# Optimization experiments

Measured on AMD Instinct MI355X. Metric: run time of the kernel, lower is better.

Reference implementation:

```python
import jax, jax.numpy as jnp
import numpy as np

NX, NY = 512, 512
DX, DY = 1e-4, 1e-4
VS = 1550.0
DT = 2.5e-8


def setup_inputs() -> dict:
    key = jax.random.key(0)
    k1, k2 = jax.random.split(key)
    sensor_data = jax.random.normal(k1, (4, 2, 128, 2048), dtype=jnp.float32)
    sensor_xy = jax.random.randint(k2, (128, 2), 0, 512, dtype=jnp.int32)
    return {"sensor_data": sensor_data, "sensor_xy": sensor_xy}


def _delay_indices(sensor_xy):
    # pixel grids, 1-indexed as in the torch code (arange(1,513))
    ix = jnp.arange(1, NX + 1, dtype=jnp.float32)[None, :, None]  # (1,Nx,1)
    iy = jnp.arange(1, NY + 1, dtype=jnp.float32)[None, None, :]  # (1,1,Ny)
    x = sensor_xy[:, 0].astype(jnp.float32)[:, None, None]        # (S,1,1)
    y = sensor_xy[:, 1].astype(jnp.float32)[:, None, None]
    dis = jnp.sqrt(((x - ix + 1.0) * DX) ** 2 + ((y - iy + 1.0) * DY) ** 2)  # (S,Nx,Ny)
    # .to(torch.long) truncates; values are non-negative so int cast matches
    return (dis / VS / DT).astype(jnp.int32).reshape(sensor_xy.shape[0], -1)  # (S, Nx*Ny)


def reference(sensor_data, sensor_xy):
    B = sensor_data.shape[0]
    S = sensor_xy.shape[0]
    t = _delay_indices(sensor_xy)                           # (S, P) int32
    data = jnp.transpose(sensor_data, (2, 0, 1, 3))         # (S, B, 2, T)

    def step(img, xs):
        t_s, d_s = xs                                       # (P,), (B,2,T)
        return img + d_s[:, :, t_s], None                   # gather + accumulate

    img0 = jnp.zeros((B, 2, NX * NY), dtype=sensor_data.dtype)
    img, _ = jax.lax.scan(step, img0, (t, data))
    return img.reshape(B, 2, NX, NY)
```

## Files before the change

kernel.cpp:

```cpp
#include <hip/hip_runtime.h>
#include <math.h>


#define NXY 512
#define S_CNT 128
#define T_CNT 2048
#define CH 8
#define CH_STRIDE (S_CNT * T_CNT)
#define NPIX (NXY * NXY)
#define TAB_BYTES (NPIX * 2)
#define CHUNK 32
#define NCHUNK (S_CNT / CHUNK)
#define WIN 64
#define PATW 24
#define PAT_STRIDE (16 * PATW)

#pragma float_control(push)
#pragma float_control(precise, on)
__device__ __forceinline__ unsigned short delay_entry(int adx, int ady) {
    const double DX32 = (double)1e-4f;
    const double R1 = (double)(float)(1.0 / 1550.0);
    const double R2 = (double)(float)(1.0 / (double)2.5e-8f);
    float dxf = (float)((double)adx * DX32);
    float dyf = (float)((double)ady * DX32);
    float a2 = (float)((double)dxf * (double)dxf);
    float b2 = (float)((double)dyf * (double)dyf);
    float sum = (float)((double)a2 + (double)b2);
    float dis = (float)sqrt((double)sum);
    float q1 = (float)((double)dis * R1);
    float q2 = (float)((double)q1 * R2);
    return (unsigned short)(int)q2;
}

__device__ __forceinline__ unsigned int bf16_rne(float f) {
    unsigned int x = __float_as_uint(f);
    return (x + 0x7fffu + ((x >> 16) & 1u)) >> 16;
}

__global__ __launch_bounds__(256) void prep4(const float* __restrict__ data,
                                             unsigned short* __restrict__ tab,
                                             uint4* __restrict__ d2b) {
    int g = blockIdx.x * 256 + threadIdx.x;
    unsigned int t01, t23;
    {
        int i0 = 4 * g;
        t01 = (unsigned int)delay_entry(i0 >> 9, i0 & 511) |
              ((unsigned int)delay_entry((i0 + 1) >> 9, (i0 + 1) & 511) << 16);
        t23 = (unsigned int)delay_entry((i0 + 2) >> 9, (i0 + 2) & 511) |
              ((unsigned int)delay_entry((i0 + 3) >> 9, (i0 + 3) & 511) << 16);
    }
    ((uint2*)tab)[g] = make_uint2(t01, t23);

    const float4* data4 = (const float4*)data;
    float4 v[CH];
#pragma unroll
    for (int ch = 0; ch < CH; ++ch) v[ch] = data4[ch * (CH_STRIDE / 4) + g];
#pragma unroll
    for (int q = 0; q < 4; ++q) {
        const float* e0 = (const float*)&v[0];
        unsigned int w0 = bf16_rne(((const float*)&v[0])[q]) | (bf16_rne(((const float*)&v[1])[q]) << 16);
        unsigned int w1 = bf16_rne(((const float*)&v[2])[q]) | (bf16_rne(((const float*)&v[3])[q]) << 16);
        unsigned int w2 = bf16_rne(((const float*)&v[4])[q]) | (bf16_rne(((const float*)&v[5])[q]) << 16);
        unsigned int w3 = bf16_rne(((const float*)&v[6])[q]) | (bf16_rne(((const float*)&v[7])[q]) << 16);
        d2b[4 * g + q] = make_uint4(w0, w1, w2, w3);
        (void)e0;
    }
}

__device__ __forceinline__ int tmin_entry(int adx, int ady) {
    return (int)delay_entry(adx, ady);
}
#pragma float_control(pop)

__device__ __forceinline__ float bflo(unsigned int u) { return __uint_as_float(u << 16); }
__device__ __forceinline__ float bfhi(unsigned int u) { return __uint_as_float(u & 0xffff0000u); }

__device__ __forceinline__ unsigned int sub16x2(unsigned int a, unsigned int t) {
    unsigned int lo = (a - t) & 0xffffu;
    unsigned int hi = ((a >> 16) - t) << 16;
    return lo | hi;
}

__global__ __launch_bounds__(256) void das_gather_ilp(const uint4* __restrict__ d2b,
                                                      const unsigned short* __restrict__ tab,
                                                      const int* __restrict__ sxy,
                                                      float* __restrict__ out) {
    __shared__ uint2 minfo[S_CNT];
    __shared__ uint2 mstage[S_CNT];
    __shared__ uint4 winb[CHUNK * WIN];
    __shared__ uint4 patb[CHUNK * 16 * 3];
    const unsigned short* pat16 = (const unsigned short*)patb;

    int tid = threadIdx.x;
    int x0 = (blockIdx.x >> 5) << 4;
    int y0 = (blockIdx.x & 31) << 4;

    if (tid < S_CNT) {
        int sxv = sxy[2 * tid];
        int syv = sxy[2 * tid + 1];
        int axm = sxv < x0 ? x0 - sxv : (sxv > x0 + 15 ? sxv - x0 - 15 : 0);
        int aym = syv < y0 ? y0 - syv : (syv > y0 + 15 ? syv - y0 - 15 : 0);
        int ay0 = aym & ~7;
        int tmin = tmin_entry(axm, aym);
        minfo[tid] = make_uint2((unsigned int)(sxv | (syv << 16)),
                                (unsigned int)(axm * PATW + ay0));
        mstage[tid] = make_uint2((unsigned int)(axm | (ay0 << 16)), (unsigned int)tmin);
    }
    __syncthreads();

    int iy = y0 | (((tid >> 6) & 1) << 3) | (tid & 7);
    int ix = x0 | ((tid >> 7) << 3) | ((tid >> 3) & 7);

    float acc[CH];
#pragma unroll
    for (int k = 0; k < CH; ++k) acc[k] = 0.0f;

    for (int c = 0; c < NCHUNK; ++c) {
        int s0 = c * CHUNK;

        {
            int lsw = tid >> 3;
            int tm = (int)mstage[s0 + lsw].y;
            const uint4* src = d2b + ((s0 + lsw) << 11) + tm;
            int e0 = tid & 7;
#pragma unroll
            for (int j = 0; j < 8; ++j)
                winb[(lsw << 6) + e0 + 8 * j] = src[e0 + 8 * j];
        }

#pragma unroll
        for (int j = 0; j < 6; ++j) {
            unsigned int idx = (unsigned int)tid + 256u * j;
            unsigned int r3 = idx / 3u;
            unsigned int cc = idx - r3 * 3u;
            unsigned int row = r3 & 15u;
            unsigned int ls = r3 >> 4;
            uint2 st = mstage[s0 + ls];
            int ax0 = (int)(st.x & 0xffffu);
            int ay0 = (int)(st.x >> 16);
            unsigned int tm = st.y;
            const uint4* src = (const uint4*)((const char*)tab +
                (((size_t)(ax0 + (int)row) << 10) + ((size_t)ay0 << 1) + ((size_t)cc << 4)));
            uint4 v = *src;
            v.x = sub16x2(v.x, tm);
            v.y = sub16x2(v.y, tm);
            v.z = sub16x2(v.z, tm);
            v.w = sub16x2(v.w, tm);
            patb[ls * 48u + row * 3u + cc] = v;
        }
        __syncthreads();

        unsigned int tw[CHUNK];
#pragma unroll
        for (int ls = 0; ls < CHUNK; ++ls) {
            uint2 mi = minfo[s0 + ls];
            int sxv = (int)(mi.x & 0xffffu);
            int syv = (int)(mi.x >> 16);
            int dxi = sxv - ix;
            int dyi = syv - iy;
            int adx = dxi < 0 ? -dxi : dxi;
            int ady = dyi < 0 ? -dyi : dyi;
            int pidx = adx * PATW + ady - (int)mi.y;
            tw[ls] = (unsigned int)pat16[ls * PAT_STRIDE + pidx];
        }

#pragma unroll
        for (int ls = 0; ls < CHUNK; ++ls) {
            uint4 w = winb[(ls << 6) + tw[ls]];
            acc[0] += bflo(w.x);
            acc[1] += bfhi(w.x);
            acc[2] += bflo(w.y);
            acc[3] += bfhi(w.y);
            acc[4] += bflo(w.z);
            acc[5] += bfhi(w.z);
            acc[6] += bflo(w.w);
            acc[7] += bfhi(w.w);
        }
        __syncthreads();
    }

    int pix = (ix << 9) | iy;
#pragma unroll
    for (int k = 0; k < CH; ++k) out[k * NPIX + pix] = acc[k];
}

#pragma float_control(push)
#pragma float_control(precise, on)
__global__ __launch_bounds__(256) void build_table(unsigned short* __restrict__ tab) {
    int idx = blockIdx.x * 256 + threadIdx.x;
    tab[idx] = delay_entry(idx >> 9, idx & 511);
}
#pragma float_control(pop)

__global__ __launch_bounds__(256) void das_main(const float* __restrict__ data,
                                                const unsigned short* __restrict__ tab,
                                                const int* __restrict__ sxy,
                                                float* __restrict__ out) {
    __shared__ int sx[S_CNT];
    __shared__ int sy[S_CNT];
    int tid = threadIdx.x;
    if (tid < S_CNT) {
        sx[tid] = sxy[2 * tid];
        sy[tid] = sxy[2 * tid + 1];
    }
    __syncthreads();
    int iy = ((blockIdx.x & 31) << 4) | (tid & 15);
    int ix = ((blockIdx.x >> 5) << 4) | (tid >> 4);
    float acc[CH];
#pragma unroll
    for (int k = 0; k < CH; ++k) acc[k] = 0.0f;
#pragma unroll 4
    for (int s = 0; s < S_CNT; ++s) {
        int dxi = sx[s] - ix;
        int dyi = sy[s] - iy;
        int adx = dxi < 0 ? -dxi : dxi;
        int ady = dyi < 0 ? -dyi : dyi;
        int t = (int)tab[(adx << 9) | ady];
        const float* p = data + (s << 11) + t;
#pragma unroll
        for (int k = 0; k < CH; ++k) acc[k] += p[(size_t)k * CH_STRIDE];
    }
    int pix = (ix << 9) | iy;
#pragma unroll
    for (int k = 0; k < CH; ++k) out[k * NPIX + pix] = acc[k];
}

extern "C" void kernel_launch(void* const* d_in, const int* in_sizes, int n_in,
                              void* d_out, int out_size, void* d_ws, size_t ws_size,
                              hipStream_t stream) {
    const float* data = (const float*)d_in[0];
    const int* sxy = (const int*)d_in[1];
    float* out = (float*)d_out;
    unsigned short* tab = (unsigned short*)d_ws;

    size_t need = (size_t)TAB_BYTES + (size_t)CH_STRIDE * 16;
    if (ws_size >= need) {
        uint4* d2b = (uint4*)((char*)d_ws + TAB_BYTES);
        prep4<<<NPIX / 1024, 256, 0, stream>>>(data, tab, d2b);
        das_gather_ilp<<<1024, 256, 0, stream>>>(d2b, tab, sxy, out);
    } else {
        build_table<<<NPIX / 256, 256, 0, stream>>>(tab);
        das_main<<<1024, 256, 0, stream>>>(data, tab, sxy, out);
    }
}
```

Baseline: 117.1 us.

## Gather sensor samples directly from global memory instead of LDS window staging

Removes the per-chunk staging of a 64-sample bf16 window per sensor into shared memory, along with the tmin offset subtraction. Each pixel now loads its delayed sample straight from the global d2b buffer, relying on L1/L2 caching. The 32-wide two-phase loop with a register array is replaced by a single loop unrolled by 4. This cuts LDS traffic, shared memory use and one write phase per chunk, and may raise occupancy. In exchange every sample becomes a scattered global load with higher latency.

Result: faster. 101.2 us (-13.6%).

```diff
diff --git a/kernel.cpp b/kernel.cpp
--- a/kernel.cpp
+++ b/kernel.cpp
@@ -11,7 +11,6 @@
 #define TAB_BYTES (NPIX * 2)
 #define CHUNK 32
 #define NCHUNK (S_CNT / CHUNK)
-#define WIN 64
 #define PATW 24
 #define PAT_STRIDE (16 * PATW)
 
@@ -57,37 +56,24 @@
     for (int ch = 0; ch < CH; ++ch) v[ch] = data4[ch * (CH_STRIDE / 4) + g];
 #pragma unroll
     for (int q = 0; q < 4; ++q) {
-        const float* e0 = (const float*)&v[0];
         unsigned int w0 = bf16_rne(((const float*)&v[0])[q]) | (bf16_rne(((const float*)&v[1])[q]) << 16);
         unsigned int w1 = bf16_rne(((const float*)&v[2])[q]) | (bf16_rne(((const float*)&v[3])[q]) << 16);
         unsigned int w2 = bf16_rne(((const float*)&v[4])[q]) | (bf16_rne(((const float*)&v[5])[q]) << 16);
         unsigned int w3 = bf16_rne(((const float*)&v[6])[q]) | (bf16_rne(((const float*)&v[7])[q]) << 16);
         d2b[4 * g + q] = make_uint4(w0, w1, w2, w3);
-        (void)e0;
-    }
-}
-
-__device__ __forceinline__ int tmin_entry(int adx, int ady) {
-    return (int)delay_entry(adx, ady);
+    }
 }
 #pragma float_control(pop)
 
 __device__ __forceinline__ float bflo(unsigned int u) { return __uint_as_float(u << 16); }
 __device__ __forceinline__ float bfhi(unsigned int u) { return __uint_as_float(u & 0xffff0000u); }
 
-__device__ __forceinline__ unsigned int sub16x2(unsigned int a, unsigned int t) {
-    unsigned int lo = (a - t) & 0xffffu;
-    unsigned int hi = ((a >> 16) - t) << 16;
-    return lo | hi;
-}
-
-__global__ __launch_bounds__(256) void das_gather_ilp(const uint4* __restrict__ d2b,
-                                                      const unsigned short* __restrict__ tab,
-                                                      const int* __restrict__ sxy,
-                                                      float* __restrict__ out) {
+__global__ __launch_bounds__(256) void das_hybrid(const uint4* __restrict__ d2b,
+                                                  const unsigned short* __restrict__ tab,
+                                                  const int* __restrict__ sxy,
+                                                  float* __restrict__ out) {
     __shared__ uint2 minfo[S_CNT];
-    __shared__ uint2 mstage[S_CNT];
-    __shared__ uint4 winb[CHUNK * WIN];
+    __shared__ unsigned int mstage[S_CNT];
     __shared__ uint4 patb[CHUNK * 16 * 3];
     const unsigned short* pat16 = (const unsigned short*)patb;
 
@@ -101,10 +87,9 @@
         int axm = sxv < x0 ? x0 - sxv : (sxv > x0 + 15 ? sxv - x0 - 15 : 0);
         int aym = syv < y0 ? y0 - syv : (syv > y0 + 15 ? syv - y0 - 15 : 0);
         int ay0 = aym & ~7;
-        int tmin = tmin_entry(axm, aym);
         minfo[tid] = make_uint2((unsigned int)(sxv | (syv << 16)),
                                 (unsigned int)(axm * PATW + ay0));
-        mstage[tid] = make_uint2((unsigned int)(axm | (ay0 << 16)), (unsigned int)tmin);
+        mstage[tid] = (unsigned int)(axm | (ay0 << 16));
     }
     __syncthreads();
 
@@ -117,16 +102,6 @@
 
     for (int c = 0; c < NCHUNK; ++c) {
         int s0 = c * CHUNK;
-
-        {
-            int lsw = tid >> 3;
-            int tm = (int)mstage[s0 + lsw].y;
-            const uint4* src = d2b + ((s0 + lsw) << 11) + tm;
-            int e0 = tid & 7;
-#pragma unroll
-            for (int j = 0; j < 8; ++j)
-                winb[(lsw << 6) + e0 + 8 * j] = src[e0 + 8 * j];
-        }
 
 #pragma unroll
         for (int j = 0; j < 6; ++j) {
@@ -135,23 +110,16 @@
             unsigned int cc = idx - r3 * 3u;
             unsigned int row = r3 & 15u;
             unsigned int ls = r3 >> 4;
-            uint2 st = mstage[s0 + ls];
-            int ax0 = (int)(st.x & 0xffffu);
-            int ay0 = (int)(st.x >> 16);
-            unsigned int tm = st.y;
+            unsigned int st = mstage[s0 + ls];
+            int ax0 = (int)(st & 0xffffu);
+            int ay0 = (int)(st >> 16);
             const uint4* src = (const uint4*)((const char*)tab +
                 (((size_t)(ax0 + (int)row) << 10) + ((size_t)ay0 << 1) + ((size_t)cc << 4)));
-            uint4 v = *src;
-            v.x = sub16x2(v.x, tm);
-            v.y = sub16x2(v.y, tm);
-            v.z = sub16x2(v.z, tm);
-            v.w = sub16x2(v.w, tm);
-            patb[ls * 48u + row * 3u + cc] = v;
+            patb[ls * 48u + row * 3u + cc] = *src;
         }
         __syncthreads();
 
-        unsigned int tw[CHUNK];
-#pragma unroll
+#pragma unroll 4
         for (int ls = 0; ls < CHUNK; ++ls) {
             uint2 mi = minfo[s0 + ls];
             int sxv = (int)(mi.x & 0xffffu);
@@ -161,12 +129,8 @@
             int adx = dxi < 0 ? -dxi : dxi;
             int ady = dyi < 0 ? -dyi : dyi;
             int pidx = adx * PATW + ady - (int)mi.y;
-            tw[ls] = (unsigned int)pat16[ls * PAT_STRIDE + pidx];
-        }
-
-#pragma unroll
-        for (int ls = 0; ls < CHUNK; ++ls) {
-            uint4 w = winb[(ls << 6) + tw[ls]];
+            int t = (int)pat16[ls * PAT_STRIDE + pidx];
+            uint4 w = d2b[((s0 + ls) << 11) + t];
             acc[0] += bflo(w.x);
             acc[1] += bfhi(w.x);
             acc[2] += bflo(w.y);
@@ -237,7 +201,7 @@
     if (ws_size >= need) {
         uint4* d2b = (uint4*)((char*)d_ws + TAB_BYTES);
         prep4<<<NPIX / 1024, 256, 0, stream>>>(data, tab, d2b);
-        das_gather_ilp<<<1024, 256, 0, stream>>>(d2b, tab, sxy, out);
+        das_hybrid<<<1024, 256, 0, stream>>>(d2b, tab, sxy, out);
     } else {
         build_table<<<NPIX / 256, 256, 0, stream>>>(tab);
         das_main<<<1024, 256, 0, stream>>>(data, tab, sxy, out);
```
